# Performance work log

Hardware: AMD Instinct MI355X
Metric: run time of the kernel (lower is better)

Reference implementation:

```python
import jax, jax.numpy as jnp
import numpy as np

N, E, H, L, G = 80000, 1280000, 64, 4, 256
ATOM_V, ATOM_F, BOND_V, BOND_F = 100, 9, 10, 3
EPS = 1e-7

def _ln(x, g, b):
    mu = jnp.mean(x, axis=-1, keepdims=True)
    var = jnp.mean((x - mu) ** 2, axis=-1, keepdims=True)
    return (x - mu) * jax.lax.rsqrt(var + 1e-5) * g + b

def setup_inputs() -> dict:
    key = jax.random.key(0)
    ks = jax.random.split(key, 16)
    inp = {}
    inp['x'] = jax.random.randint(ks[0], (N, ATOM_F), 0, ATOM_V)
    inp['edge_attr'] = jax.random.randint(ks[1], (E, BOND_F), 0, BOND_V)
    inp['edge_index'] = jax.random.randint(ks[2], (2, E), 0, N)
    inp['batch'] = jnp.sort(jax.random.randint(ks[3], (N,), 0, G))
    s = 0.05
    inp['atom_emb'] = jax.random.normal(ks[4], (ATOM_F * ATOM_V, H)) * s
    inp['bond_emb'] = jax.random.normal(ks[5], (BOND_F * BOND_V, H)) * s
    inp['t'] = jnp.ones((L,))
    inp['W1'] = jax.random.normal(ks[6], (L, H, 2 * H)) * s
    inp['b1'] = jnp.zeros((L, 2 * H))
    inp['ln1_g'] = jnp.ones((L, 2 * H))
    inp['ln1_b'] = jnp.zeros((L, 2 * H))
    inp['W2'] = jax.random.normal(ks[7], (L, 2 * H, H)) * s
    inp['b2'] = jnp.zeros((L, H))
    inp['norm_g'] = jnp.ones((L, H))
    inp['norm_b'] = jnp.zeros((L, H))
    return inp

def reference(x, edge_attr, edge_index, batch, atom_emb, bond_emb, t,
              W1, b1, ln1_g, ln1_b, W2, b2, norm_g, norm_b):
    src, dst = edge_index[0], edge_index[1]
    # encoders: sum of per-feature embeddings (flattened tables with offsets)
    xn = jnp.sum(atom_emb[x + jnp.arange(ATOM_F) * ATOM_V], axis=1)   # [N,H]
    ea = jnp.sum(bond_emb[edge_attr + jnp.arange(BOND_F) * BOND_V], axis=1)  # [E,H]

    def genconv(h, l):
        msg = jax.nn.relu(h[src] + ea) + EPS                    # [E,H]
        m = msg * t[l]
        mx = jax.ops.segment_max(m, dst, num_segments=N)        # per-dst, per-channel
        ex = jnp.exp(m - mx[dst])
        den = jax.ops.segment_sum(ex, dst, num_segments=N)
        alpha = ex / (den[dst] + 1e-16)
        agg = jax.ops.segment_sum(alpha * msg, dst, num_segments=N)
        o = agg + h                                             # root add
        mid = jax.nn.relu(_ln(o @ W1[l] + b1[l], ln1_g[l], ln1_b[l]))
        return mid @ W2[l] + b2[l]

    cur = genconv(xn, 0)
    for l in range(1, L):  # res+ blocks: x + conv(act(norm(x)))  (dropout inactive in eval)
        hh = jax.nn.relu(_ln(cur, norm_g[l], norm_b[l]))
        cur = cur + genconv(hh, l)
    out = jax.nn.relu(_ln(cur, norm_g[0], norm_b[0]))
    # per-graph mean pooling
    sums = jax.ops.segment_sum(out, batch, num_segments=G)
    cnts = jax.ops.segment_sum(jnp.ones((out.shape[0],), out.dtype), batch, num_segments=G)
    return sums / jnp.maximum(cnts, 1.0)[:, None]
```

## Files before the change

### kernel.cpp

```cpp
#include <hip/hip_runtime.h>
#include <hip/hip_bf16.h>
#include <hip/hip_fp16.h>

#define NN 80000
#define NE 1280000
#define NL 4
#define NG 256

typedef __attribute__((ext_vector_type(8))) _Float16 half8;
typedef __attribute__((ext_vector_type(4))) float f32x4;

__device__ __forceinline__ float wave_sum(float v) {
    for (int off = 32; off; off >>= 1) v += __shfl_xor(v, off, 64);
    return v;
}

__global__ void k_count(const int* __restrict__ idx, int* __restrict__ cnt) {
    int e = blockIdx.x * 256 + threadIdx.x;
    if (e < NE) atomicAdd(&cnt[idx[e]], 1);
}

__global__ void k_scan1(const int* __restrict__ in, int* __restrict__ out,
                        int* __restrict__ bsum, int n) {
    __shared__ int ws[4];
    int i = blockIdx.x * 256 + threadIdx.x;
    int v = (i < n) ? in[i] : 0;
    int lane = threadIdx.x & 63, w = threadIdx.x >> 6;
    for (int off = 1; off < 64; off <<= 1) {
        int t = __shfl_up(v, off, 64);
        if (lane >= off) v += t;
    }
    if (lane == 63) ws[w] = v;
    __syncthreads();
    if (threadIdx.x == 0) {
        int acc = 0;
        for (int k = 0; k < 4; k++) { int t = ws[k]; ws[k] = acc; acc += t; }
    }
    __syncthreads();
    v += ws[w];
    if (i < n) out[i] = v;
    if (threadIdx.x == 255) bsum[blockIdx.x] = v;
}

__global__ void k_scan2(int* __restrict__ bsum, int nb) {
    __shared__ int ws[4];
    __shared__ int carry;
    if (threadIdx.x == 0) carry = 0;
    __syncthreads();
    for (int base = 0; base < nb; base += 256) {
        int i = base + threadIdx.x;
        int v = (i < nb) ? bsum[i] : 0;
        int lane = threadIdx.x & 63, w = threadIdx.x >> 6;
        for (int off = 1; off < 64; off <<= 1) {
            int t = __shfl_up(v, off, 64);
            if (lane >= off) v += t;
        }
        if (lane == 63) ws[w] = v;
        __syncthreads();
        if (threadIdx.x == 0) {
            int acc = carry;
            for (int k = 0; k < 4; k++) { int t = ws[k]; ws[k] = acc; acc += t; }
            carry = acc;
        }
        __syncthreads();
        v += ws[w];
        if (i < nb) bsum[i] = v;
        __syncthreads();
    }
}

__global__ void k_scan3(int* __restrict__ rowptr, const int* __restrict__ bsum, int n) {
    int i = blockIdx.x * 256 + threadIdx.x;
    if (i < n) {
        int off = (blockIdx.x > 0) ? bsum[blockIdx.x - 1] : 0;
        rowptr[1 + i] += off;
    }
    if (i == 0 && blockIdx.x == 0) rowptr[0] = 0;
}

__global__ void k_fill(const int* __restrict__ src, const int* __restrict__ dst,
                       const int* __restrict__ eattr, const int* __restrict__ rowptr,
                       int* __restrict__ wofs, int* __restrict__ csr32) {
    int e = blockIdx.x * 256 + threadIdx.x;
    if (e >= NE) return;
    int d = dst[e];
    int pos = rowptr[d] + atomicAdd(&wofs[d], 1);
    int a0 = eattr[e * 3], a1 = eattr[e * 3 + 1], a2 = eattr[e * 3 + 2];
    csr32[pos] = (src[e] << 10) | (a0 + a1 * 10 + a2 * 100);
}

__global__ void k_comb(const float* __restrict__ bond_emb, __half* __restrict__ comb) {
    int wid = (blockIdx.x * 256 + threadIdx.x) >> 6;
    int lane = threadIdx.x & 63;
    if (wid >= 1000) return;
    int a0 = wid % 10, a1 = (wid / 10) % 10, a2 = wid / 100;
    comb[wid * 64 + lane] = __float2half(bond_emb[a0 * 64 + lane] +
                                         bond_emb[(10 + a1) * 64 + lane] +
                                         bond_emb[(20 + a2) * 64 + lane]);
}

__global__ void k_atom(const int* __restrict__ x, const float* __restrict__ atom_emb,
                       __half* __restrict__ xn) {
    int wid = (blockIdx.x * 256 + threadIdx.x) >> 6;
    int lane = threadIdx.x & 63;
    if (wid >= NN) return;
    float acc = 0.f;
#pragma unroll
    for (int f = 0; f < 9; f++) {
        int idx = x[wid * 9 + f] + f * 100;
        acc += atom_emb[idx * 64 + lane];
    }
    xn[wid * 64 + lane] = __float2half(acc);
}

__global__ void k_packw(const float* __restrict__ W1, const float* __restrict__ W2,
                        __half* __restrict__ w1t, __half* __restrict__ w2t) {
    int i = blockIdx.x * 256 + threadIdx.x;
    if (i >= NL * 8192) return;
    int l = i >> 13, r = i & 8191;
    int n1 = r >> 6, k1 = r & 63;
    w1t[i] = __float2half(W1[(l * 64 + k1) * 128 + n1]);
    int n2 = r >> 7, k2 = r & 127;
    w2t[i] = __float2half(W2[(l * 128 + k2) * 64 + n2]);
}

__global__ __launch_bounds__(256) void k_agg(
    const __half* __restrict__ hin, const int* __restrict__ rowptr,
    const int* __restrict__ csr32, const __half* __restrict__ comb,
    const float* __restrict__ t, int l, __half* __restrict__ o) {
    int wid = blockIdx.x * 4 + (threadIdx.x >> 6);
    int lane = threadIdx.x & 63;
    float tl = t[l];
    long oi = (long)wid * 64 + lane;
    float hroot = __half2float(hin[oi]);
    int rs = rowptr[wid], re = rowptr[wid + 1];
    float den = 0.f, num = 0.f;
#pragma unroll 4
    for (int p = rs; p < re; ++p) {
        int v = csr32[p];
        float h = __half2float(hin[(long)(v >> 10) * 64 + lane]);
        float c = __half2float(comb[(v & 1023) * 64 + lane]);
        float m = fmaxf(h + c, 0.f) + 1e-7f;
        float e = __expf(m * tl);
        den += e;
        num = fmaf(e, m, num);
    }
    o[oi] = __float2half(num / (den + 1e-16f) + hroot);
}

__global__ __launch_bounds__(256) void k_mlp(
    const __half* __restrict__ o, int l,
    const __half* __restrict__ w1t, const __half* __restrict__ w2t,
    const float* __restrict__ b1, const float* __restrict__ g1,
    const float* __restrict__ bb1, const float* __restrict__ b2,
    float* __restrict__ cur, int residual,
    __half* __restrict__ hh, const float* __restrict__ ng, const float* __restrict__ nbv) {
    __shared__ __half midL[4][16][136];
    int w = threadIdx.x >> 6, lane = threadIdx.x & 63;
    int node0 = blockIdx.x * 64 + w * 16;
    int lm = lane & 15, lh = lane >> 4;

    const __half* ob = o + (long)(node0 + lm) * 64 + lh * 8;
    half8 a0 = *(const half8*)(ob);
    half8 a1 = *(const half8*)(ob + 32);
    const __half* w1b = w1t + l * 8192 + lm * 64 + lh * 8;
    f32x4 acc[8];
#pragma unroll
    for (int nb = 0; nb < 8; ++nb) {
        f32x4 c = {0.f, 0.f, 0.f, 0.f};
        half8 b0 = *(const half8*)(w1b + nb * 1024);
        half8 bx = *(const half8*)(w1b + nb * 1024 + 32);
        c = __builtin_amdgcn_mfma_f32_16x16x32_f16(a0, b0, c, 0, 0, 0);
        c = __builtin_amdgcn_mfma_f32_16x16x32_f16(a1, bx, c, 0, 0, 0);
        acc[nb] = c;
    }

    float bv[8], gv[8], bbv[8];
#pragma unroll
    for (int nb = 0; nb < 8; ++nb) {
        int n = l * 128 + nb * 16 + lm;
        bv[nb] = b1[n]; gv[nb] = g1[n]; bbv[nb] = bb1[n];
    }
    float ps[4] = {0.f, 0.f, 0.f, 0.f};
#pragma unroll
    for (int nb = 0; nb < 8; ++nb)
#pragma unroll
        for (int r = 0; r < 4; ++r) { acc[nb][r] += bv[nb]; ps[r] += acc[nb][r]; }
#pragma unroll
    for (int r = 0; r < 4; ++r) {
        for (int off = 1; off < 16; off <<= 1) ps[r] += __shfl_xor(ps[r], off, 64);
        ps[r] *= (1.f / 128.f);
    }
    float pv[4] = {0.f, 0.f, 0.f, 0.f};
#pragma unroll
    for (int nb = 0; nb < 8; ++nb)
#pragma unroll
        for (int r = 0; r < 4; ++r) { float d = acc[nb][r] - ps[r]; pv[r] = fmaf(d, d, pv[r]); }
#pragma unroll
    for (int r = 0; r < 4; ++r) {
        for (int off = 1; off < 16; off <<= 1) pv[r] += __shfl_xor(pv[r], off, 64);
        pv[r] = rsqrtf(pv[r] * (1.f / 128.f) + 1e-5f);
    }
#pragma unroll
    for (int nb = 0; nb < 8; ++nb)
#pragma unroll
        for (int r = 0; r < 4; ++r) {
            float m = fmaxf((acc[nb][r] - ps[r]) * pv[r] * gv[nb] + bbv[nb], 0.f);
            midL[w][lh * 4 + r][nb * 16 + lm] = __float2half(m);
        }

    const __half* mrow = &midL[w][lm][lh * 8];
    const __half* w2b = w2t + l * 8192 + lm * 128 + lh * 8;
    f32x4 acc2[4];
#pragma unroll
    for (int nb = 0; nb < 4; ++nb) acc2[nb] = (f32x4){0.f, 0.f, 0.f, 0.f};
#pragma unroll
    for (int kb = 0; kb < 4; ++kb) {
        half8 a = *(const half8*)(mrow + kb * 32);
#pragma unroll
        for (int nb = 0; nb < 4; ++nb) {
            half8 b = *(const half8*)(w2b + nb * 2048 + kb * 32);
            acc2[nb] = __builtin_amdgcn_mfma_f32_16x16x32_f16(a, b, acc2[nb], 0, 0, 0);
        }
    }

    float b2v[4], cps[4] = {0.f, 0.f, 0.f, 0.f};
    float cv[4][4];
#pragma unroll
    for (int nb = 0; nb < 4; ++nb) b2v[nb] = b2[l * 64 + nb * 16 + lm];
#pragma unroll
    for (int nb = 0; nb < 4; ++nb)
#pragma unroll
        for (int r = 0; r < 4; ++r) {
            long ci = (long)(node0 + lh * 4 + r) * 64 + nb * 16 + lm;
            float z = acc2[nb][r] + b2v[nb] + (residual ? cur[ci] : 0.f);
            cur[ci] = z;
            cv[nb][r] = z;
            cps[r] += z;
        }
    if (hh) {
        float gn[4], bn[4], mu[4], rv[4];
        float pvv[4] = {0.f, 0.f, 0.f, 0.f};
#pragma unroll
        for (int nb = 0; nb < 4; ++nb) { gn[nb] = ng[nb * 16 + lm]; bn[nb] = nbv[nb * 16 + lm]; }
#pragma unroll
        for (int r = 0; r < 4; ++r) {
            float s = cps[r];
            for (int off = 1; off < 16; off <<= 1) s += __shfl_xor(s, off, 64);
            mu[r] = s * (1.f / 64.f);
        }
#pragma unroll
        for (int nb = 0; nb < 4; ++nb)
#pragma unroll
            for (int r = 0; r < 4; ++r) { float d = cv[nb][r] - mu[r]; pvv[r] = fmaf(d, d, pvv[r]); }
#pragma unroll
        for (int r = 0; r < 4; ++r) {
            float s = pvv[r];
            for (int off = 1; off < 16; off <<= 1) s += __shfl_xor(s, off, 64);
            rv[r] = rsqrtf(s * (1.f / 64.f) + 1e-5f);
        }
#pragma unroll
        for (int nb = 0; nb < 4; ++nb)
#pragma unroll
            for (int r = 0; r < 4; ++r) {
                long ci = (long)(node0 + lh * 4 + r) * 64 + nb * 16 + lm;
                hh[ci] = __float2half(fmaxf((cv[nb][r] - mu[r]) * rv[r] * gn[nb] + bn[nb], 0.f));
            }
    }
}

__global__ void k_bounds(const int* __restrict__ batch, int* __restrict__ gstart) {
    int i = blockIdx.x * 256 + threadIdx.x;
    if (i >= NN) return;
    int b = batch[i];
    if (i == 0) {
        for (int g = 0; g <= b; ++g) gstart[g] = 0;
    } else {
        int pb = batch[i - 1];
        for (int g = pb + 1; g <= b; ++g) gstart[g] = i;
    }
    if (i == NN - 1) {
        for (int g = b + 1; g <= NG; ++g) gstart[g] = NN;
    }
}

__global__ __launch_bounds__(1024) void k_pool2(
    const float* __restrict__ cur, const int* __restrict__ gstart,
    const float* __restrict__ g, const float* __restrict__ b,
    float* __restrict__ out) {
    int gi = blockIdx.x;
    int lane = threadIdx.x & 63, w = threadIdx.x >> 6;
    int s = gstart[gi], e = gstart[gi + 1];
    float gg = g[lane], bb = b[lane];
    float acc = 0.f;
    for (int n = s + w; n < e; n += 16) {
        float v = cur[(long)n * 64 + lane];
        float mu = wave_sum(v) * (1.f / 64.f);
        float d = v - mu;
        float var = wave_sum(d * d) * (1.f / 64.f);
        acc += fmaxf(d * rsqrtf(var + 1e-5f) * gg + bb, 0.f);
    }
    __shared__ float sh[16][64];
    sh[w][lane] = acc;
    __syncthreads();
    if (w == 0) {
        float tot = 0.f;
#pragma unroll
        for (int k = 0; k < 16; ++k) tot += sh[k][lane];
        out[gi * 64 + lane] = tot / fmaxf((float)(e - s), 1.f);
    }
}

extern "C" void kernel_launch(void* const* d_in, const int* in_sizes, int n_in,
                              void* d_out, int out_size, void* d_ws, size_t ws_size,
                              hipStream_t stream) {
    (void)in_sizes; (void)n_in; (void)out_size; (void)ws_size;
    const int* x         = (const int*)d_in[0];
    const int* edge_attr = (const int*)d_in[1];
    const int* src       = (const int*)d_in[2];
    const int* dst       = src + NE;
    const int* batch     = (const int*)d_in[3];
    const float* atom_emb = (const float*)d_in[4];
    const float* bond_emb = (const float*)d_in[5];
    const float* t        = (const float*)d_in[6];
    const float* W1       = (const float*)d_in[7];
    const float* b1       = (const float*)d_in[8];
    const float* g1       = (const float*)d_in[9];
    const float* bb1      = (const float*)d_in[10];
    const float* W2       = (const float*)d_in[11];
    const float* b2       = (const float*)d_in[12];
    const float* norm_g   = (const float*)d_in[13];
    const float* norm_b   = (const float*)d_in[14];
    float* out = (float*)d_out;

    size_t off = 0;
    auto alloc = [&](size_t bytes) {
        void* p = (char*)d_ws + off;
        off += (bytes + 255) & ~(size_t)255;
        return p;
    };
    int*    count  = (int*)alloc((size_t)NN * 4);
    int*    wofs   = (int*)alloc((size_t)NN * 4);
    int*    rowptr = (int*)alloc((size_t)(NN + 1) * 4);
    int*    bsum   = (int*)alloc(4096);
    int*    csr32  = (int*)alloc((size_t)NE * 4);
    __half* comb   = (__half*)alloc(1000 * 64 * 2);
    __half* xnH    = (__half*)alloc((size_t)NN * 64 * 2);
    __half* hhH    = (__half*)alloc((size_t)NN * 64 * 2);
    __half* oH     = (__half*)alloc((size_t)NN * 64 * 2);
    float*  cur    = (float*)alloc((size_t)NN * 64 * 4);
    int*    gstart = (int*)alloc((size_t)(NG + 1) * 4);
    __half* w1t    = (__half*)alloc((size_t)NL * 8192 * 2);
    __half* w2t    = (__half*)alloc((size_t)NL * 8192 * 2);

    hipMemsetAsync(count, 0, (size_t)NN * 4, stream);
    hipMemsetAsync(wofs, 0, (size_t)NN * 4, stream);

    const int EB = (NE + 255) / 256;
    const int SB = (NN + 255) / 256;
    const int WB = (NN * 64 + 255) / 256;

    k_count<<<EB, 256, 0, stream>>>(dst, count);
    k_scan1<<<SB, 256, 0, stream>>>(count, rowptr + 1, bsum, NN);
    k_scan2<<<1, 256, 0, stream>>>(bsum, SB);
    k_scan3<<<SB, 256, 0, stream>>>(rowptr, bsum, NN);
    k_fill<<<EB, 256, 0, stream>>>(src, dst, edge_attr, rowptr, wofs, csr32);
    k_comb<<<(1000 * 64 + 255) / 256, 256, 0, stream>>>(bond_emb, comb);
    k_atom<<<WB, 256, 0, stream>>>(x, atom_emb, xnH);
    k_bounds<<<SB, 256, 0, stream>>>(batch, gstart);
    k_packw<<<(NL * 8192 + 255) / 256, 256, 0, stream>>>(W1, W2, w1t, w2t);

    const int AB = NN / 4;
    const int MBK = NN / 64;
    for (int l = 0; l < NL; ++l) {
        const __half* hin = (l == 0) ? xnH : hhH;
        __half* hh_out = (l < NL - 1) ? hhH : nullptr;
        const float* ngp = norm_g + (l + 1 < NL ? (l + 1) * 64 : 0);
        const float* nbp = norm_b + (l + 1 < NL ? (l + 1) * 64 : 0);
        k_agg<<<AB, 256, 0, stream>>>(hin, rowptr, csr32, comb, t, l, oH);
        k_mlp<<<MBK, 256, 0, stream>>>(oH, l, w1t, w2t, b1, g1, bb1, b2,
                                       cur, l > 0, hh_out, ngp, nbp);
    }
    k_pool2<<<NG, 1024, 0, stream>>>(cur, gstart, norm_g, norm_b, out);
}
```

Measured before the change: 541.4 us.

## Bucket edges before CSR fill and split aggregation across edge pairs

Measured after the change: 1.198 ms. 121% more time.

```diff
diff --git a/kernel.cpp b/kernel.cpp
--- a/kernel.cpp
+++ b/kernel.cpp
@@ -6,6 +6,7 @@
 #define NE 1280000
 #define NL 4
 #define NG 256
+#define NB 313
 
 typedef __attribute__((ext_vector_type(8))) _Float16 half8;
 typedef __attribute__((ext_vector_type(4))) float f32x4;
@@ -15,9 +16,21 @@
     return v;
 }
 
-__global__ void k_count(const int* __restrict__ idx, int* __restrict__ cnt) {
+__global__ void k_histB(const int* __restrict__ dst, int* __restrict__ cnt,
+                        int* __restrict__ gh) {
+    __shared__ int lh[NB];
+    for (int i = threadIdx.x; i < NB; i += 256) lh[i] = 0;
+    __syncthreads();
     int e = blockIdx.x * 256 + threadIdx.x;
-    if (e < NE) atomicAdd(&cnt[idx[e]], 1);
+    int d = 0;
+    if (e < NE) {
+        d = dst[e];
+        atomicAdd(&cnt[d], 1);
+        atomicAdd(&lh[d >> 8], 1);
+    }
+    __syncthreads();
+    for (int i = threadIdx.x; i < NB; i += 256)
+        if (lh[i]) atomicAdd(&gh[i], lh[i]);
 }
 
 __global__ void k_scan1(const int* __restrict__ in, int* __restrict__ out,
@@ -78,15 +91,25 @@
     if (i == 0 && blockIdx.x == 0) rowptr[0] = 0;
 }
 
-__global__ void k_fill(const int* __restrict__ src, const int* __restrict__ dst,
-                       const int* __restrict__ eattr, const int* __restrict__ rowptr,
-                       int* __restrict__ wofs, int* __restrict__ csr32) {
+__global__ void k_scatB(const int* __restrict__ src, const int* __restrict__ dst,
+                        const int* __restrict__ eattr, const int* __restrict__ ghist,
+                        int* __restrict__ bofs, int2* __restrict__ ebuf) {
     int e = blockIdx.x * 256 + threadIdx.x;
     if (e >= NE) return;
-    int d = dst[e];
-    int pos = rowptr[d] + atomicAdd(&wofs[d], 1);
+    int d = dst[e], b = d >> 8;
+    int base = (b ? ghist[b - 1] : 0);
+    int pos = base + atomicAdd(&bofs[b], 1);
     int a0 = eattr[e * 3], a1 = eattr[e * 3 + 1], a2 = eattr[e * 3 + 2];
-    csr32[pos] = (src[e] << 10) | (a0 + a1 * 10 + a2 * 100);
+    ebuf[pos] = make_int2((src[e] << 10) | (a0 + a1 * 10 + a2 * 100), d);
+}
+
+__global__ void k_fill2(const int2* __restrict__ ebuf, const int* __restrict__ rowptr,
+                        int* __restrict__ wofs, int* __restrict__ csr32) {
+    int i = blockIdx.x * 256 + threadIdx.x;
+    if (i >= NE) return;
+    int2 v = ebuf[i];
+    int pos = rowptr[v.y] + atomicAdd(&wofs[v.y], 1);
+    csr32[pos] = v.x;
 }
 
 __global__ void k_comb(const float* __restrict__ bond_emb, __half* __restrict__ comb) {
@@ -124,28 +147,35 @@
     w2t[i] = __float2half(W2[(l * 128 + k2) * 64 + n2]);
 }
 
-__global__ __launch_bounds__(256) void k_agg(
+__global__ __launch_bounds__(256) void k_agg2(
     const __half* __restrict__ hin, const int* __restrict__ rowptr,
     const int* __restrict__ csr32, const __half* __restrict__ comb,
     const float* __restrict__ t, int l, __half* __restrict__ o) {
     int wid = blockIdx.x * 4 + (threadIdx.x >> 6);
     int lane = threadIdx.x & 63;
+    int half = lane >> 5;
+    int ch = (lane & 31) + blockIdx.y * 32;
     float tl = t[l];
-    long oi = (long)wid * 64 + lane;
+    long oi = (long)wid * 64 + ch;
     float hroot = __half2float(hin[oi]);
     int rs = rowptr[wid], re = rowptr[wid + 1];
+    int nIt = (re - rs + 1) >> 1;
     float den = 0.f, num = 0.f;
 #pragma unroll 4
-    for (int p = rs; p < re; ++p) {
-        int v = csr32[p];
-        float h = __half2float(hin[(long)(v >> 10) * 64 + lane]);
-        float c = __half2float(comb[(v & 1023) * 64 + lane]);
+    for (int i = 0; i < nIt; ++i) {
+        int p = rs + 2 * i + half;
+        bool valid = p < re;
+        int v = csr32[valid ? p : rs];
+        float h = __half2float(hin[(long)(v >> 10) * 64 + ch]);
+        float c = __half2float(comb[(v & 1023) * 64 + ch]);
         float m = fmaxf(h + c, 0.f) + 1e-7f;
-        float e = __expf(m * tl);
+        float e = valid ? __expf(m * tl) : 0.f;
         den += e;
         num = fmaf(e, m, num);
     }
-    o[oi] = __float2half(num / (den + 1e-16f) + hroot);
+    den += __shfl_xor(den, 32, 64);
+    num += __shfl_xor(num, 32, 64);
+    if (half == 0) o[oi] = __float2half(num / (den + 1e-16f) + hroot);
 }
 
 __global__ __launch_bounds__(256) void k_mlp(
@@ -343,7 +373,10 @@
     int*    wofs   = (int*)alloc((size_t)NN * 4);
     int*    rowptr = (int*)alloc((size_t)(NN + 1) * 4);
     int*    bsum   = (int*)alloc(4096);
+    int*    gHist  = (int*)alloc((size_t)NB * 4);
+    int*    bofs   = (int*)alloc((size_t)NB * 4);
     int*    csr32  = (int*)alloc((size_t)NE * 4);
+    int2*   ebuf   = (int2*)alloc((size_t)NE * 8);
     __half* comb   = (__half*)alloc(1000 * 64 * 2);
     __half* xnH    = (__half*)alloc((size_t)NN * 64 * 2);
     __half* hhH    = (__half*)alloc((size_t)NN * 64 * 2);
@@ -355,29 +388,33 @@
 
     hipMemsetAsync(count, 0, (size_t)NN * 4, stream);
     hipMemsetAsync(wofs, 0, (size_t)NN * 4, stream);
+    hipMemsetAsync(gHist, 0, (size_t)NB * 4, stream);
+    hipMemsetAsync(bofs, 0, (size_t)NB * 4, stream);
 
     const int EB = (NE + 255) / 256;
     const int SB = (NN + 255) / 256;
     const int WB = (NN * 64 + 255) / 256;
 
-    k_count<<<EB, 256, 0, stream>>>(dst, count);
+    k_histB<<<EB, 256, 0, stream>>>(dst, count, gHist);
     k_scan1<<<SB, 256, 0, stream>>>(count, rowptr + 1, bsum, NN);
     k_scan2<<<1, 256, 0, stream>>>(bsum, SB);
     k_scan3<<<SB, 256, 0, stream>>>(rowptr, bsum, NN);
-    k_fill<<<EB, 256, 0, stream>>>(src, dst, edge_attr, rowptr, wofs, csr32);
+    k_scan2<<<1, 256, 0, stream>>>(gHist, NB);
+    k_scatB<<<EB, 256, 0, stream>>>(src, dst, edge_attr, gHist, bofs, ebuf);
+    k_fill2<<<EB, 256, 0, stream>>>(ebuf, rowptr, wofs, csr32);
     k_comb<<<(1000 * 64 + 255) / 256, 256, 0, stream>>>(bond_emb, comb);
     k_atom<<<WB, 256, 0, stream>>>(x, atom_emb, xnH);
     k_bounds<<<SB, 256, 0, stream>>>(batch, gstart);
     k_packw<<<(NL * 8192 + 255) / 256, 256, 0, stream>>>(W1, W2, w1t, w2t);
 
-    const int AB = NN / 4;
+    const dim3 AB(NN / 4, 2);
     const int MBK = NN / 64;
     for (int l = 0; l < NL; ++l) {
         const __half* hin = (l == 0) ? xnH : hhH;
         __half* hh_out = (l < NL - 1) ? hhH : nullptr;
         const float* ngp = norm_g + (l + 1 < NL ? (l + 1) * 64 : 0);
         const float* nbp = norm_b + (l + 1 < NL ? (l + 1) * 64 : 0);
-        k_agg<<<AB, 256, 0, stream>>>(hin, rowptr, csr32, comb, t, l, oH);
+        k_agg2<<<AB, 256, 0, stream>>>(hin, rowptr, csr32, comb, t, l, oH);
         k_mlp<<<MBK, 256, 0, stream>>>(oH, l, w1t, w2t, b1, g1, bb1, b2,
                                        cur, l > 0, hh_out, ngp, nbp);
     }
```

## Process two nodes per wave with half2 gathers and merge setup kernels

Applied to the files above, without the earlier changes.

Result: faster. 489.6 us (-9.6%).

```diff
diff --git a/kernel.cpp b/kernel.cpp
--- a/kernel.cpp
+++ b/kernel.cpp
@@ -89,14 +89,37 @@
     csr32[pos] = (src[e] << 10) | (a0 + a1 * 10 + a2 * 100);
 }
 
-__global__ void k_comb(const float* __restrict__ bond_emb, __half* __restrict__ comb) {
-    int wid = (blockIdx.x * 256 + threadIdx.x) >> 6;
-    int lane = threadIdx.x & 63;
-    if (wid >= 1000) return;
-    int a0 = wid % 10, a1 = (wid / 10) % 10, a2 = wid / 100;
-    comb[wid * 64 + lane] = __float2half(bond_emb[a0 * 64 + lane] +
-                                         bond_emb[(10 + a1) * 64 + lane] +
-                                         bond_emb[(20 + a2) * 64 + lane]);
+__global__ void k_prep(const float* __restrict__ bond_emb, __half* __restrict__ comb,
+                       const float* __restrict__ W1, const float* __restrict__ W2,
+                       __half* __restrict__ w1t, __half* __restrict__ w2t,
+                       const int* __restrict__ batch, int* __restrict__ gstart) {
+    int idx = blockIdx.x * 256 + threadIdx.x;
+    if (idx < NN) {
+        int b = batch[idx];
+        if (idx == 0) {
+            for (int g = 0; g <= b; ++g) gstart[g] = 0;
+        } else {
+            int pb = batch[idx - 1];
+            for (int g = pb + 1; g <= b; ++g) gstart[g] = idx;
+        }
+        if (idx == NN - 1) {
+            for (int g = b + 1; g <= NG; ++g) gstart[g] = NN;
+        }
+    }
+    if (idx < 64000) {
+        int wid = idx >> 6, lane = idx & 63;
+        int a0 = wid % 10, a1 = (wid / 10) % 10, a2 = wid / 100;
+        comb[wid * 64 + lane] = __float2half(bond_emb[a0 * 64 + lane] +
+                                             bond_emb[(10 + a1) * 64 + lane] +
+                                             bond_emb[(20 + a2) * 64 + lane]);
+    }
+    if (idx < NL * 8192) {
+        int l = idx >> 13, r = idx & 8191;
+        int n1 = r >> 6, k1 = r & 63;
+        w1t[idx] = __float2half(W1[(l * 64 + k1) * 128 + n1]);
+        int n2 = r >> 7, k2 = r & 127;
+        w2t[idx] = __float2half(W2[(l * 128 + k2) * 64 + n2]);
+    }
 }
 
 __global__ void k_atom(const int* __restrict__ x, const float* __restrict__ atom_emb,
@@ -113,39 +136,41 @@
     xn[wid * 64 + lane] = __float2half(acc);
 }
 
-__global__ void k_packw(const float* __restrict__ W1, const float* __restrict__ W2,
-                        __half* __restrict__ w1t, __half* __restrict__ w2t) {
-    int i = blockIdx.x * 256 + threadIdx.x;
-    if (i >= NL * 8192) return;
-    int l = i >> 13, r = i & 8191;
-    int n1 = r >> 6, k1 = r & 63;
-    w1t[i] = __float2half(W1[(l * 64 + k1) * 128 + n1]);
-    int n2 = r >> 7, k2 = r & 127;
-    w2t[i] = __float2half(W2[(l * 128 + k2) * 64 + n2]);
-}
-
-__global__ __launch_bounds__(256) void k_agg(
+__global__ __launch_bounds__(256) void k_agg3(
     const __half* __restrict__ hin, const int* __restrict__ rowptr,
     const int* __restrict__ csr32, const __half* __restrict__ comb,
     const float* __restrict__ t, int l, __half* __restrict__ o) {
-    int wid = blockIdx.x * 4 + (threadIdx.x >> 6);
+    int w = blockIdx.x * 4 + (threadIdx.x >> 6);
     int lane = threadIdx.x & 63;
+    int half = lane >> 5, lc = lane & 31;
+    int node = w * 2 + half;
     float tl = t[l];
-    long oi = (long)wid * 64 + lane;
-    float hroot = __half2float(hin[oi]);
-    int rs = rowptr[wid], re = rowptr[wid + 1];
-    float den = 0.f, num = 0.f;
+    const __half2* hin2 = (const __half2*)hin;
+    const __half2* comb2 = (const __half2*)comb;
+    long oi2 = (long)node * 32 + lc;
+    __half2 hr2 = hin2[oi2];
+    int rs0 = rowptr[w * 2], mid = rowptr[w * 2 + 1], re1 = rowptr[w * 2 + 2];
+    int base = half ? mid : rs0;
+    int cnt = half ? (re1 - mid) : (mid - rs0);
+    int cmax = max(mid - rs0, re1 - mid);
+    float den0 = 0.f, den1 = 0.f, num0 = 0.f, num1 = 0.f;
 #pragma unroll 4
-    for (int p = rs; p < re; ++p) {
-        int v = csr32[p];
-        float h = __half2float(hin[(long)(v >> 10) * 64 + lane]);
-        float c = __half2float(comb[(v & 1023) * 64 + lane]);
-        float m = fmaxf(h + c, 0.f) + 1e-7f;
-        float e = __expf(m * tl);
-        den += e;
-        num = fmaf(e, m, num);
-    }
-    o[oi] = __float2half(num / (den + 1e-16f) + hroot);
+    for (int i = 0; i < cmax; ++i) {
+        bool valid = i < cnt;
+        int v = csr32[valid ? base + i : 0];
+        __half2 h2 = hin2[(long)(v >> 10) * 32 + lc];
+        __half2 c2 = comb2[(v & 1023) * 32 + lc];
+        __half2 s2 = __hadd2(h2, c2);
+        float m0 = fmaxf(__low2float(s2), 0.f) + 1e-7f;
+        float m1 = fmaxf(__high2float(s2), 0.f) + 1e-7f;
+        float e0 = valid ? __expf(m0 * tl) : 0.f;
+        float e1 = valid ? __expf(m1 * tl) : 0.f;
+        den0 += e0; num0 = fmaf(e0, m0, num0);
+        den1 += e1; num1 = fmaf(e1, m1, num1);
+    }
+    float r0 = num0 / (den0 + 1e-16f) + __low2float(hr2);
+    float r1 = num1 / (den1 + 1e-16f) + __high2float(hr2);
+    ((__half2*)o)[oi2] = __floats2half2_rn(r0, r1);
 }
 
 __global__ __launch_bounds__(256) void k_mlp(
@@ -266,21 +291,6 @@
                 long ci = (long)(node0 + lh * 4 + r) * 64 + nb * 16 + lm;
                 hh[ci] = __float2half(fmaxf((cv[nb][r] - mu[r]) * rv[r] * gn[nb] + bn[nb], 0.f));
             }
-    }
-}
-
-__global__ void k_bounds(const int* __restrict__ batch, int* __restrict__ gstart) {
-    int i = blockIdx.x * 256 + threadIdx.x;
-    if (i >= NN) return;
-    int b = batch[i];
-    if (i == 0) {
-        for (int g = 0; g <= b; ++g) gstart[g] = 0;
-    } else {
-        int pb = batch[i - 1];
-        for (int g = pb + 1; g <= b; ++g) gstart[g] = i;
-    }
-    if (i == NN - 1) {
-        for (int g = b + 1; g <= NG; ++g) gstart[g] = NN;
     }
 }
 
@@ -365,19 +375,17 @@
     k_scan2<<<1, 256, 0, stream>>>(bsum, SB);
     k_scan3<<<SB, 256, 0, stream>>>(rowptr, bsum, NN);
     k_fill<<<EB, 256, 0, stream>>>(src, dst, edge_attr, rowptr, wofs, csr32);
-    k_comb<<<(1000 * 64 + 255) / 256, 256, 0, stream>>>(bond_emb, comb);
+    k_prep<<<SB, 256, 0, stream>>>(bond_emb, comb, W1, W2, w1t, w2t, batch, gstart);
     k_atom<<<WB, 256, 0, stream>>>(x, atom_emb, xnH);
-    k_bounds<<<SB, 256, 0, stream>>>(batch, gstart);
-    k_packw<<<(NL * 8192 + 255) / 256, 256, 0, stream>>>(W1, W2, w1t, w2t);
-
-    const int AB = NN / 4;
+
+    const int AB = NN / 8;
     const int MBK = NN / 64;
     for (int l = 0; l < NL; ++l) {
         const __half* hin = (l == 0) ? xnH : hhH;
         __half* hh_out = (l < NL - 1) ? hhH : nullptr;
         const float* ngp = norm_g + (l + 1 < NL ? (l + 1) * 64 : 0);
         const float* nbp = norm_b + (l + 1 < NL ? (l + 1) * 64 : 0);
-        k_agg<<<AB, 256, 0, stream>>>(hin, rowptr, csr32, comb, t, l, oH);
+        k_agg3<<<AB, 256, 0, stream>>>(hin, rowptr, csr32, comb, t, l, oH);
         k_mlp<<<MBK, 256, 0, stream>>>(oH, l, w1t, w2t, b1, g1, bb1, b2,
                                        cur, l > 0, hh_out, ngp, nbp);
     }
```
